# Optimization experiments

Hardware: AMD Instinct MI355X
Metric: run time of the kernel (lower is better)

The kernel has to match this reference:

```python
import jax, jax.numpy as jnp
import numpy as np

B, C, H, W = 8, 512, 64, 64
R = 16
CQK = C // R  # 32


def setup_inputs() -> dict:
    key = jax.random.key(0)
    kx, kq, kk, kv = jax.random.split(key, 4)
    x = jax.random.normal(kx, (B, C, H, W), dtype=jnp.float32)
    # Conv1d with kernel_size=1, bias=False == matmul over channel dim
    Wq = jax.random.normal(kq, (CQK, C), dtype=jnp.float32) * (1.0 / np.sqrt(C))
    Wk = jax.random.normal(kk, (CQK, C), dtype=jnp.float32) * (1.0 / np.sqrt(C))
    Wv = jax.random.normal(kv, (C, C), dtype=jnp.float32) * (1.0 / np.sqrt(C))
    return {"x": x, "Wq": Wq, "Wk": Wk, "Wv": Wv}


def reference(x, Wq, Wk, Wv):
    b, c, h, w = x.shape
    xf = x.reshape(b, c, h * w)                 # [b, c, n]
    q = jnp.einsum('dc,bcn->bdn', Wq, xf)       # [b, c/r, n]
    k = jnp.einsum('dc,bcn->bdn', Wk, xf)       # [b, c/r, n]
    attn = jax.nn.softmax(jnp.einsum('bdm,bdn->bmn', q, k), axis=-1)  # [b, n, n]
    v = jnp.einsum('dc,bcn->bdn', Wv, xf)       # [b, c, n]
    out = jnp.einsum('bcm,bmn->bcn', v, attn)   # [b, c, n]
    return out.reshape(b, c, h, w)
```

## Files before the change

kernel.cpp:

```cpp
#include <hip/hip_runtime.h>
#include <hip/hip_bf16.h>


typedef __attribute__((ext_vector_type(8))) short s16x8;
typedef __attribute__((ext_vector_type(4))) float f32x4;

#define MFMA16(a, b, c) __builtin_amdgcn_mfma_f32_16x16x32_bf16((a), (b), (c), 0, 0, 0)

__device__ __forceinline__ ushort f2bf(float f) {
  union { float f; unsigned u; } v; v.f = f;
  return (ushort)((v.u + 0x8000u) >> 16);
}
__device__ __forceinline__ unsigned pack_bf16(float lo, float hi) {
  union { float f; unsigned u; } a, b; a.f = lo; b.f = hi;
  return __builtin_amdgcn_perm(b.u + 0x8000u, a.u + 0x8000u, 0x07060302u);
}
__device__ __forceinline__ float fexp2(float x) { return __builtin_amdgcn_exp2f(x); }

__device__ __forceinline__ void chunk_barrier() {
  asm volatile("s_waitcnt lgkmcnt(0)" ::: "memory");
  __builtin_amdgcn_s_barrier();
  __builtin_amdgcn_sched_barrier(0);
}

__global__ void k_cvt_w(const float* __restrict__ Wq, const float* __restrict__ Wk,
                        const float* __restrict__ Wv, ushort* __restrict__ Wqb,
                        ushort* __restrict__ Wkb, ushort* __restrict__ Wvb) {
  int i = blockIdx.x * 256 + threadIdx.x;
  if (i < 262144) Wvb[i] = f2bf(Wv[i]);
  else if (i < 278528) Wqb[i - 262144] = f2bf(Wq[i - 262144] * 1.4426950408889634f);
  else if (i < 294912) Wkb[i - 278528] = f2bf(Wk[i - 278528]);
}

__global__ __launch_bounds__(256, 2) void k_proj(const float* __restrict__ x,
                                                 const ushort* __restrict__ Wqb,
                                                 const ushort* __restrict__ Wkb,
                                                 const ushort* __restrict__ Wvb,
                                                 ushort* __restrict__ qb,
                                                 ushort* __restrict__ kb,
                                                 ushort* __restrict__ vb) {
  const int b = blockIdx.y, n0 = blockIdx.x * 64;
  const int t = threadIdx.x;
  const int lane = t & 63, w = t >> 6;
  const int quad = lane >> 4, l15 = lane & 15;

  __shared__ __align__(16) ushort XB[64 * 512];
  __shared__ uint U[2][2][32][17];

  const float* x_b = x + (size_t)b * 512 * 4096;

  auto ldX = [&](int s, float4& fa, float4& fb) {
    const int c0s = s * 32;
    const float* p = x_b + (size_t)(c0s + (t >> 4)) * 4096 + n0 + (t & 15) * 4;
    fa = *(const float4*)p;
    fb = *(const float4*)(p + (size_t)16 * 4096);
  };
  auto packU = [&](int ub, const float4& fa, const float4& fb) {
    const int cr = t >> 4, c4 = t & 15;
    U[ub][0][cr][c4] = pack_bf16(fa.x, fa.y);
    U[ub][1][cr][c4] = pack_bf16(fa.z, fa.w);
    U[ub][0][cr + 16][c4] = pack_bf16(fb.x, fb.y);
    U[ub][1][cr + 16][c4] = pack_bf16(fb.z, fb.w);
  };
  auto phase2 = [&](int ub, int s) {
    const int n = t & 63, gl = t >> 6;
    const int h = (n >> 1) & 1, c4 = n >> 2;
    const uint sel = (n & 1) ? 0x07060302u : 0x05040100u;
    uint o[4];
#pragma unroll
    for (int j = 0; j < 4; ++j) {
      uint ua = U[ub][h][gl * 8 + 2 * j][c4];
      uint ubv = U[ub][h][gl * 8 + 2 * j + 1][c4];
      o[j] = __builtin_amdgcn_perm(ubv, ua, sel);
    }
    const int gfull = s * 4 + gl;
    const int gsw = gfull ^ (n & 7);
    *(uint4*)((char*)XB + n * 1024 + gsw * 16) = *(uint4*)o;
  };

  float4 fa0, fb0, fa1, fb1;
  ldX(0, fa0, fb0);
  packU(0, fa0, fb0);
  ldX(1, fa1, fb1);
  __syncthreads();
#pragma unroll
  for (int s = 0; s < 16; s += 2) {
    phase2(0, s);
    if (s < 14) ldX(s + 2, fa0, fb0);
    packU(1, fa1, fb1);
    __syncthreads();
    phase2(1, s + 1);
    if (s < 14) {
      packU(0, fa0, fb0);
      ldX(s + 3, fa1, fb1);
    }
    __syncthreads();
  }

  const ushort* Wqk = (w < 2) ? (Wqb + (size_t)(w * 16 + l15) * 512)
                              : (Wkb + (size_t)((w - 2) * 16 + l15) * 512);

  f32x4 accv[8][4], accqk[4];
#pragma unroll
  for (int i = 0; i < 8; ++i)
#pragma unroll
    for (int nt = 0; nt < 4; ++nt) accv[i][nt] = {0.f, 0.f, 0.f, 0.f};
#pragma unroll
  for (int nt = 0; nt < 4; ++nt) accqk[nt] = {0.f, 0.f, 0.f, 0.f};

  const char* XBb = (const char*)XB;
  for (int k0 = 0; k0 < 512; k0 += 32) {
    s16x8 bx[4];
#pragma unroll
    for (int nt = 0; nt < 4; ++nt) {
      const int nl = nt * 16 + l15;
      bx[nt] = *(const s16x8*)(XBb + nl * 1024 + ((((k0 >> 3) + quad) ^ (nl & 7)) << 4));
    }
#pragma unroll
    for (int i = 0; i < 8; ++i) {
      s16x8 av = *(const s16x8*)(Wvb + (size_t)((8 * w + i) * 16 + l15) * 512 + k0 + quad * 8);
#pragma unroll
      for (int nt = 0; nt < 4; ++nt) accv[i][nt] = MFMA16(bx[nt], av, accv[i][nt]);
    }
    s16x8 aqk = *(const s16x8*)(Wqk + k0 + quad * 8);
#pragma unroll
    for (int nt = 0; nt < 4; ++nt) accqk[nt] = MFMA16(aqk, bx[nt], accqk[nt]);
  }

  ushort* vb_b = vb + (size_t)b * 512 * 4096;
#pragma unroll
  for (int i = 0; i < 8; ++i)
#pragma unroll
    for (int nt = 0; nt < 4; ++nt) {
      ushort4 u;
      u.x = f2bf(accv[i][nt][0]); u.y = f2bf(accv[i][nt][1]);
      u.z = f2bf(accv[i][nt][2]); u.w = f2bf(accv[i][nt][3]);
      *(ushort4*)(vb_b + (size_t)((8 * w + i) * 16 + l15) * 4096 + n0 + nt * 16 + quad * 4) = u;
    }

  ushort* qk_out = (w < 2) ? (qb + (size_t)b * 4096 * 32) : (kb + (size_t)b * 4096 * 32);
#pragma unroll
  for (int nt = 0; nt < 4; ++nt) {
    ushort4 u;
    u.x = f2bf(accqk[nt][0]); u.y = f2bf(accqk[nt][1]);
    u.z = f2bf(accqk[nt][2]); u.w = f2bf(accqk[nt][3]);
    *(ushort4*)(qk_out + (size_t)(n0 + nt * 16 + l15) * 32 + (w & 1) * 16 + quad * 4) = u;
  }
}

__global__ __launch_bounds__(256) void k_pass1(const ushort* __restrict__ qb,
                                               const ushort* __restrict__ kb,
                                               float* __restrict__ Lneg) {
  const int b = blockIdx.y, mt = blockIdx.x;
  const int lane = threadIdx.x & 63, w = threadIdx.x >> 6;
  const int quad = lane >> 4, l15 = lane & 15;
  const int m = mt * 64 + w * 16;
  const ushort* qb_b = qb + (size_t)b * 4096 * 32;
  const ushort* kb_b = kb + (size_t)b * 4096 * 32;
  const s16x8 aqf = *(const s16x8*)(qb_b + (size_t)(m + l15) * 32 + quad * 8);
  float ps[4] = {0.f, 0.f, 0.f, 0.f};
  const f32x4 zf = {0.f, 0.f, 0.f, 0.f};
  for (int n0 = 0; n0 < 4096; n0 += 64) {
#pragma unroll
    for (int nt = 0; nt < 4; ++nt) {
      s16x8 bk = *(const s16x8*)(kb_b + (size_t)(n0 + nt * 16 + l15) * 32 + quad * 8);
      f32x4 s = MFMA16(aqf, bk, zf);
#pragma unroll
      for (int r = 0; r < 4; ++r) ps[r] += fexp2(s[r]);
    }
  }
  for (int off = 1; off < 16; off <<= 1)
#pragma unroll
    for (int r = 0; r < 4; ++r) ps[r] += __shfl_xor(ps[r], off, 64);
  if (l15 == 0)
#pragma unroll
    for (int r = 0; r < 4; ++r)
      Lneg[(size_t)b * 4096 + m + quad * 4 + r] = -log2f(ps[r]);
}

__global__ __launch_bounds__(512, 2) void k_pass2(const ushort* __restrict__ qb,
                                                  const ushort* __restrict__ kb,
                                                  const ushort* __restrict__ vb,
                                                  const float* __restrict__ Lneg,
                                                  float* __restrict__ out) {
  const int blk = blockIdx.x;
  const int b = blk & 7, ntb = blk >> 3;
  const int nbase = ntb * 128;
  const int lane = threadIdx.x & 63, w = threadIdx.x >> 6;
  const int quad = lane >> 4, l15 = lane & 15;
  const int cbase = w * 64;
  const int swz = l15 & 7;
  const int Mw = w >> 1;
  const int Tb = (w & 1) * 4;

  __shared__ __align__(16) ushort PT[2][128 * 64];

  const ushort* qb_b = qb + (size_t)b * 4096 * 32;
  const ushort* kb_b = kb + (size_t)b * 4096 * 32;
  const ushort* vb_b = vb + (size_t)b * 512 * 4096;
  const float* L_b = Lneg + (size_t)b * 4096;

  s16x8 kf[4];
#pragma unroll
  for (int i = 0; i < 4; ++i)
    kf[i] = *(const s16x8*)(kb_b + (size_t)(nbase + (Tb + i) * 16 + l15) * 32 + quad * 8);

  f32x4 acc[4][8];
#pragma unroll
  for (int ci = 0; ci < 4; ++ci)
#pragma unroll
    for (int nt = 0; nt < 8; ++nt) acc[ci][nt] = {0.f, 0.f, 0.f, 0.f};

  s16x8 aqp;
  float4 l4p;
  s16x8 va0[4], va1[4];

  auto loadQ = [&](int chunk) {
    const int m0 = chunk * 64;
    aqp = *(const s16x8*)(qb_b + (size_t)(m0 + Mw * 16 + l15) * 32 + quad * 8);
    l4p = *(const float4*)(L_b + m0 + Mw * 16 + quad * 4);
  };
  auto loadV0 = [&](int chunk) {
    const int m0 = chunk * 64;
#pragma unroll
    for (int ci = 0; ci < 4; ++ci)
      va0[ci] = *(const s16x8*)(vb_b + (size_t)(cbase + ci * 16 + l15) * 4096 + m0 + quad * 8);
  };
  auto loadV1 = [&](int chunk) {
    const int m0 = chunk * 64;
#pragma unroll
    for (int ci = 0; ci < 4; ++ci)
      va1[ci] = *(const s16x8*)(vb_b + (size_t)(cbase + ci * 16 + l15) * 4096 + m0 + 32 + quad * 8);
  };
  auto produce_tile = [&](int buf, int i) {
    char* Pw = (char*)&PT[buf][0];
    const int T = Tb + i;
    f32x4 cin; cin.x = l4p.x; cin.y = l4p.y; cin.z = l4p.z; cin.w = l4p.w;
    f32x4 s = MFMA16(aqp, kf[i], cin);
    uint2 u;
    u.x = pack_bf16(fexp2(s.x), fexp2(s.y));
    u.y = pack_bf16(fexp2(s.z), fexp2(s.w));
    const int row = T * 16 + l15;
    const int gran = (2 * Mw + (quad >> 1)) ^ swz;
    *(uint2*)(Pw + row * 128 + gran * 16 + (quad & 1) * 8) = u;
  };

  loadQ(0);
#pragma unroll
  for (int i = 0; i < 4; ++i) produce_tile(0, i);
  loadQ(1);
  loadV0(0);
  loadV1(0);

  for (int chunk = 0; chunk < 64; ++chunk) {
    const int buf = chunk & 1;
    chunk_barrier();
    const char* P = (const char*)&PT[buf][0];
    s16x8 pg[8];
#pragma unroll
    for (int nt = 0; nt < 8; ++nt)
      pg[nt] = *(const s16x8*)(P + (nt * 16 + l15) * 128 + (quad ^ swz) * 16);
#pragma unroll
    for (int i = 0; i < 4; ++i) produce_tile(buf ^ 1, i);
    if (chunk < 62) loadQ(chunk + 2);
    __builtin_amdgcn_s_setprio(1);
    s16x8 rr[8];
#pragma unroll
    for (int nt = 0; nt < 8; ++nt) {
#pragma unroll
      for (int ci = 0; ci < 4; ++ci) acc[ci][nt] = MFMA16(va0[ci], pg[nt], acc[ci][nt]);
      rr[nt] = *(const s16x8*)(P + (nt * 16 + l15) * 128 + ((4 + quad) ^ swz) * 16);
    }
    __builtin_amdgcn_s_setprio(0);
    if (chunk < 63) loadV0(chunk + 1);
    __builtin_amdgcn_s_setprio(1);
#pragma unroll
    for (int nt = 0; nt < 8; ++nt)
#pragma unroll
      for (int ci = 0; ci < 4; ++ci) acc[ci][nt] = MFMA16(va1[ci], rr[nt], acc[ci][nt]);
    __builtin_amdgcn_s_setprio(0);
    if (chunk < 63) loadV1(chunk + 1);
  }

  float* out_b = out + (size_t)b * 512 * 4096;
#pragma unroll
  for (int ci = 0; ci < 4; ++ci)
#pragma unroll
    for (int nt = 0; nt < 8; ++nt) {
      const int n = nbase + nt * 16 + l15;
      const int c0 = cbase + ci * 16 + quad * 4;
#pragma unroll
      for (int r = 0; r < 4; ++r) out_b[(size_t)(c0 + r) * 4096 + n] = acc[ci][nt][r];
    }
}

extern "C" void kernel_launch(void* const* d_in, const int* in_sizes, int n_in,
                              void* d_out, int out_size, void* d_ws, size_t ws_size,
                              hipStream_t stream) {
  const float* x  = (const float*)d_in[0];
  const float* Wq = (const float*)d_in[1];
  const float* Wk = (const float*)d_in[2];
  const float* Wv = (const float*)d_in[3];
  float* out = (float*)d_out;

  char* ws = (char*)d_ws;
  ushort* vb  = (ushort*)(ws + 0);
  ushort* qb  = (ushort*)(ws + 33554432);
  ushort* kb  = (ushort*)(ws + 35651584);
  ushort* Wvb = (ushort*)(ws + 37748736);
  ushort* Wqb = (ushort*)(ws + 38273024);
  ushort* Wkb = (ushort*)(ws + 38305792);
  float*  Lrs = (float*)(ws + 38338560);

  hipLaunchKernelGGL(k_cvt_w, dim3(1152), dim3(256), 0, stream, Wq, Wk, Wv, Wqb, Wkb, Wvb);
  hipLaunchKernelGGL(k_proj, dim3(64, 8), dim3(256), 0, stream, x, Wqb, Wkb, Wvb, qb, kb, vb);
  hipLaunchKernelGGL(k_pass1, dim3(64, 8), dim3(256), 0, stream, qb, kb, Lrs);
  hipLaunchKernelGGL(k_pass2, dim3(256), dim3(512), 0, stream, qb, kb, vb, Lrs, out);
}
```

Baseline: 321.5 us.

## Double the key chunk per barrier in pass2 and pipeline P reads in halves

The pass2 loop now handles 128 keys per iteration instead of 64. Each wave produces two Q tiles per step into a P buffer that is twice as large, 64 KB across the two buffers. This halves the number of block barriers. P fragments are now read from LDS in groups of four interleaved with the MFMA batches, and V loads are spread across four quarter-stages of each iteration. The larger LDS footprint may limit the two-blocks-per-CU occupancy target, and the longer unrolled body raises register pressure.

Result: slower. 328.5 us (+2.2%).

```diff
diff --git a/kernel.cpp b/kernel.cpp
--- a/kernel.cpp
+++ b/kernel.cpp
@@ -193,7 +193,7 @@
   const int Mw = w >> 1;
   const int Tb = (w & 1) * 4;
 
-  __shared__ __align__(16) ushort PT[2][128 * 64];
+  __shared__ __align__(16) ushort PT[2][128 * 128];
 
   const ushort* qb_b = qb + (size_t)b * 4096 * 32;
   const ushort* kb_b = kb + (size_t)b * 4096 * 32;
@@ -211,75 +211,117 @@
 #pragma unroll
     for (int nt = 0; nt < 8; ++nt) acc[ci][nt] = {0.f, 0.f, 0.f, 0.f};
 
-  s16x8 aqp;
-  float4 l4p;
+  s16x8 aqp[2];
+  float4 l4p[2];
   s16x8 va0[4], va1[4];
 
-  auto loadQ = [&](int chunk) {
-    const int m0 = chunk * 64;
-    aqp = *(const s16x8*)(qb_b + (size_t)(m0 + Mw * 16 + l15) * 32 + quad * 8);
-    l4p = *(const float4*)(L_b + m0 + Mw * 16 + quad * 4);
-  };
-  auto loadV0 = [&](int chunk) {
-    const int m0 = chunk * 64;
+  auto loadQ = [&](int c2) {
+    const int m0 = c2 * 128;
+#pragma unroll
+    for (int j = 0; j < 2; ++j) {
+      const int M = 2 * Mw + j;
+      aqp[j] = *(const s16x8*)(qb_b + (size_t)(m0 + M * 16 + l15) * 32 + quad * 8);
+      l4p[j] = *(const float4*)(L_b + m0 + M * 16 + quad * 4);
+    }
+  };
+  auto loadV = [&](s16x8* va, int c2, int q) {
+    const int m0 = c2 * 128 + q * 32;
 #pragma unroll
     for (int ci = 0; ci < 4; ++ci)
-      va0[ci] = *(const s16x8*)(vb_b + (size_t)(cbase + ci * 16 + l15) * 4096 + m0 + quad * 8);
-  };
-  auto loadV1 = [&](int chunk) {
-    const int m0 = chunk * 64;
-#pragma unroll
-    for (int ci = 0; ci < 4; ++ci)
-      va1[ci] = *(const s16x8*)(vb_b + (size_t)(cbase + ci * 16 + l15) * 4096 + m0 + 32 + quad * 8);
-  };
-  auto produce_tile = [&](int buf, int i) {
+      va[ci] = *(const s16x8*)(vb_b + (size_t)(cbase + ci * 16 + l15) * 4096 + m0 + quad * 8);
+  };
+  auto produce_tile = [&](int buf, int j, int i) {
     char* Pw = (char*)&PT[buf][0];
+    const int M = 2 * Mw + j;
     const int T = Tb + i;
-    f32x4 cin; cin.x = l4p.x; cin.y = l4p.y; cin.z = l4p.z; cin.w = l4p.w;
-    f32x4 s = MFMA16(aqp, kf[i], cin);
+    f32x4 cin; cin.x = l4p[j].x; cin.y = l4p[j].y; cin.z = l4p[j].z; cin.w = l4p[j].w;
+    f32x4 s = MFMA16(aqp[j], kf[i], cin);
     uint2 u;
     u.x = pack_bf16(fexp2(s.x), fexp2(s.y));
     u.y = pack_bf16(fexp2(s.z), fexp2(s.w));
     const int row = T * 16 + l15;
-    const int gran = (2 * Mw + (quad >> 1)) ^ swz;
-    *(uint2*)(Pw + row * 128 + gran * 16 + (quad & 1) * 8) = u;
+    const int gran = (2 * M + (quad >> 1)) ^ swz;
+    *(uint2*)(Pw + row * 256 + gran * 16 + (quad & 1) * 8) = u;
+  };
+  auto rdP4 = [&](s16x8* d, int buf, int q, int ntb4) {
+    const char* P = (const char*)&PT[buf][0];
+#pragma unroll
+    for (int k = 0; k < 4; ++k) {
+      const int row = (ntb4 + k) * 16 + l15;
+      d[k] = *(const s16x8*)(P + row * 256 + (((q * 4 + quad) ^ swz) << 4));
+    }
   };
 
   loadQ(0);
 #pragma unroll
-  for (int i = 0; i < 4; ++i) produce_tile(0, i);
+  for (int j = 0; j < 2; ++j)
+#pragma unroll
+    for (int i = 0; i < 4; ++i) produce_tile(0, j, i);
   loadQ(1);
-  loadV0(0);
-  loadV1(0);
-
-  for (int chunk = 0; chunk < 64; ++chunk) {
-    const int buf = chunk & 1;
+  loadV(va0, 0, 0);
+  loadV(va1, 0, 1);
+
+  for (int c2 = 0; c2 < 32; ++c2) {
+    const int buf = c2 & 1;
     chunk_barrier();
-    const char* P = (const char*)&PT[buf][0];
-    s16x8 pg[8];
-#pragma unroll
-    for (int nt = 0; nt < 8; ++nt)
-      pg[nt] = *(const s16x8*)(P + (nt * 16 + l15) * 128 + (quad ^ swz) * 16);
-#pragma unroll
-    for (int i = 0; i < 4; ++i) produce_tile(buf ^ 1, i);
-    if (chunk < 62) loadQ(chunk + 2);
+    s16x8 pg[4], rr[4];
+    rdP4(pg, buf, 0, 0);
+#pragma unroll
+    for (int j = 0; j < 2; ++j)
+#pragma unroll
+      for (int i = 0; i < 4; ++i) produce_tile(buf ^ 1, j, i);
+    if (c2 < 30) loadQ(c2 + 2);
     __builtin_amdgcn_s_setprio(1);
-    s16x8 rr[8];
-#pragma unroll
-    for (int nt = 0; nt < 8; ++nt) {
-#pragma unroll
-      for (int ci = 0; ci < 4; ++ci) acc[ci][nt] = MFMA16(va0[ci], pg[nt], acc[ci][nt]);
-      rr[nt] = *(const s16x8*)(P + (nt * 16 + l15) * 128 + ((4 + quad) ^ swz) * 16);
-    }
+    rdP4(rr, buf, 0, 4);
+#pragma unroll
+    for (int k = 0; k < 4; ++k)
+#pragma unroll
+      for (int ci = 0; ci < 4; ++ci) acc[ci][k] = MFMA16(va0[ci], pg[k], acc[ci][k]);
+    rdP4(pg, buf, 1, 0);
+#pragma unroll
+    for (int k = 0; k < 4; ++k)
+#pragma unroll
+      for (int ci = 0; ci < 4; ++ci) acc[ci][4 + k] = MFMA16(va0[ci], rr[k], acc[ci][4 + k]);
     __builtin_amdgcn_s_setprio(0);
-    if (chunk < 63) loadV0(chunk + 1);
+    loadV(va0, c2, 2);
     __builtin_amdgcn_s_setprio(1);
-#pragma unroll
-    for (int nt = 0; nt < 8; ++nt)
-#pragma unroll
-      for (int ci = 0; ci < 4; ++ci) acc[ci][nt] = MFMA16(va1[ci], rr[nt], acc[ci][nt]);
+    rdP4(rr, buf, 1, 4);
+#pragma unroll
+    for (int k = 0; k < 4; ++k)
+#pragma unroll
+      for (int ci = 0; ci < 4; ++ci) acc[ci][k] = MFMA16(va1[ci], pg[k], acc[ci][k]);
+    rdP4(pg, buf, 2, 0);
+#pragma unroll
+    for (int k = 0; k < 4; ++k)
+#pragma unroll
+      for (int ci = 0; ci < 4; ++ci) acc[ci][4 + k] = MFMA16(va1[ci], rr[k], acc[ci][4 + k]);
     __builtin_amdgcn_s_setprio(0);
-    if (chunk < 63) loadV1(chunk + 1);
+    loadV(va1, c2, 3);
+    __builtin_amdgcn_s_setprio(1);
+    rdP4(rr, buf, 2, 4);
+#pragma unroll
+    for (int k = 0; k < 4; ++k)
+#pragma unroll
+      for (int ci = 0; ci < 4; ++ci) acc[ci][k] = MFMA16(va0[ci], pg[k], acc[ci][k]);
+    rdP4(pg, buf, 3, 0);
+#pragma unroll
+    for (int k = 0; k < 4; ++k)
+#pragma unroll
+      for (int ci = 0; ci < 4; ++ci) acc[ci][4 + k] = MFMA16(va0[ci], rr[k], acc[ci][4 + k]);
+    __builtin_amdgcn_s_setprio(0);
+    if (c2 < 31) loadV(va0, c2 + 1, 0);
+    __builtin_amdgcn_s_setprio(1);
+    rdP4(rr, buf, 3, 4);
+#pragma unroll
+    for (int k = 0; k < 4; ++k)
+#pragma unroll
+      for (int ci = 0; ci < 4; ++ci) acc[ci][k] = MFMA16(va1[ci], pg[k], acc[ci][k]);
+#pragma unroll
+    for (int k = 0; k < 4; ++k)
+#pragma unroll
+      for (int ci = 0; ci < 4; ++ci) acc[ci][4 + k] = MFMA16(va1[ci], rr[k], acc[ci][4 + k]);
+    __builtin_amdgcn_s_setprio(0);
+    if (c2 < 31) loadV(va1, c2 + 1, 1);
   }
 
   float* out_b = out + (size_t)b * 512 * 4096;
```
